# Optimization experiments

Hardware: AMD Instinct MI355X
Metric: run time of the kernel (lower is better)

The kernel has to match this reference:

```python
import jax, jax.numpy as jnp
import numpy as np
import math

B, M, DM = 8, 512, 1024
H, DH = 16, 64
DFF = 4096
RA, RF, RO = 32, 384, 384
EPS = 1e-12  # BERT LayerNorm eps


def layernorm(x, g, b):
    mu = jnp.mean(x, axis=-1, keepdims=True)
    var = jnp.mean(jnp.square(x - mu), axis=-1, keepdims=True)
    return (x - mu) * jax.lax.rsqrt(var + EPS) * g + b


def setup_inputs() -> dict:
    key = jax.random.key(0)
    ks = jax.random.split(key, 24)
    s = 0.02
    inp = {
        "x": jax.random.normal(ks[0], (B, M, DM), jnp.float32),
        "mask": jnp.zeros((B, M), jnp.float32),  # additive attention mask
        "Pq": jax.random.normal(ks[1], (H, DM, RA), jnp.float32) * s,
        "Vq": jax.random.normal(ks[2], (H, RA, DH), jnp.float32) * s,
        "Pk": jax.random.normal(ks[3], (H, DM, RA), jnp.float32) * s,
        "Vk": jax.random.normal(ks[4], (H, RA, DH), jnp.float32) * s,
        "Pv": jax.random.normal(ks[5], (H, DM, RA), jnp.float32) * s,
        "Vv": jax.random.normal(ks[6], (H, RA, DH), jnp.float32) * s,
        "bq": jax.random.normal(ks[7], (H, DH), jnp.float32) * s,
        "bk": jax.random.normal(ks[8], (H, DH), jnp.float32) * s,
        "bv": jax.random.normal(ks[9], (H, DH), jnp.float32) * s,
        "Uo": jax.random.normal(ks[10], (DM, RO), jnp.float32) * s,
        "Vo": jax.random.normal(ks[11], (RO, DM), jnp.float32) * s,
        "bo_attn": jax.random.normal(ks[12], (DM,), jnp.float32) * s,
        "U1": jax.random.normal(ks[13], (DM, RF), jnp.float32) * s,
        "V1": jax.random.normal(ks[14], (RF, DFF), jnp.float32) * s,
        "b1": jax.random.normal(ks[15], (DFF,), jnp.float32) * s,
        "U2": jax.random.normal(ks[16], (DFF, RF), jnp.float32) * s,
        "V2": jax.random.normal(ks[17], (RF, DM), jnp.float32) * s,
        "b2": jax.random.normal(ks[18], (DM,), jnp.float32) * s,
        "ln1_g": jnp.ones((DM,), jnp.float32),
        "ln1_b": jnp.zeros((DM,), jnp.float32),
        "ln2_g": jnp.ones((DM,), jnp.float32),
        "ln2_b": jnp.zeros((DM,), jnp.float32),
    }
    return inp


def reference(x, mask, Pq, Vq, Pk, Vk, Pv, Vv, bq, bk, bv,
              Uo, Vo, bo_attn, U1, V1, b1, U2, V2, b2,
              ln1_g, ln1_b, ln2_g, ln2_b):
    b_, m_, dm = x.shape
    h = Pq.shape[0]
    dh = dm // h
    # low-rank per-head projections: x -> [B,H,M,R] -> [B,H,M,dh]
    q = jnp.einsum('bmd,hdr->bhmr', x, Pq)
    k = jnp.einsum('bmd,hdr->bhmr', x, Pk)
    v = jnp.einsum('bmd,hdr->bhmr', x, Pv)
    Q = jnp.einsum('bhmr,hrd->bhmd', q, Vq) + bq[None, :, None, :]
    K = jnp.einsum('bhmr,hrd->bhmd', k, Vk) + bk[None, :, None, :]
    V = jnp.einsum('bhmr,hrd->bhmd', v, Vv) + bv[None, :, None, :]
    # scaled dot-product attention (flash_svd_attention equivalent)
    scores = jnp.einsum('bhmd,bhnd->bhmn', Q, K) / math.sqrt(dh)
    scores = scores + mask[:, None, None, :]
    probs = jax.nn.softmax(scores, axis=-1)
    attn = jnp.einsum('bhmn,bhnd->bhmd', probs, V)  # [B,H,M,dh]
    attn = attn.transpose(0, 2, 1, 3).reshape(b_, m_, dm)
    # low-rank output projection + residual + LN
    x1 = layernorm(x + (attn @ Uo) @ Vo + bo_attn, ln1_g, ln1_b)
    # flashsvd_ffn_v1 equivalent: gelu((x1 @ U1) @ V1 + b1) @ U2 @ V2 + b2
    mid = x1 @ U1
    hdn = jax.nn.gelu(mid @ V1 + b1, approximate=False)
    y = (hdn @ U2) @ V2 + b2
    out = layernorm(x1 + y, ln2_g, ln2_b)
    return out
```

## Files before the change

kernel.cpp:

```cpp
#include <hip/hip_runtime.h>
#include <math.h>

typedef __attribute__((ext_vector_type(8))) short short8;
typedef __attribute__((ext_vector_type(4))) float floatx4;

__device__ inline unsigned short f2bf(float f){
    union { float f; unsigned u; } v; v.f = f;
    unsigned r = v.u + 0x7fffu + ((v.u >> 16) & 1u);
    return (unsigned short)(r >> 16);
}
__device__ inline float bf2f(unsigned short b){
    union { unsigned u; float f; } v; v.u = ((unsigned)b) << 16;
    return v.f;
}
__device__ inline unsigned short to_bf(float f){ return f2bf(f); }
__device__ inline unsigned short to_bf(unsigned short u){ return u; }

#define GLD_LDS16(g, l) __builtin_amdgcn_global_load_lds( \
    (const __attribute__((address_space(1))) void*)(g),   \
    (__attribute__((address_space(3))) void*)(l), 16, 0, 0)

__global__ __launch_bounds__(256) void cast_kernel(const float* __restrict__ s,
                                                   unsigned short* __restrict__ d){
    int i = (blockIdx.x*256 + threadIdx.x)*4;
    float4 v = *(const float4*)(s+i);
    ushort4 o; o.x=f2bf(v.x); o.y=f2bf(v.y); o.z=f2bf(v.z); o.w=f2bf(v.w);
    *(ushort4*)(d+i) = o;
}

__global__ __launch_bounds__(256) void reduce4_kernel(
    const float* __restrict__ p, unsigned short* __restrict__ o, long mn){
    long i = ((long)blockIdx.x*256 + threadIdx.x)*4;
    float4 a = *(const float4*)(p+i);
    float4 b = *(const float4*)(p+mn+i);
    float4 c = *(const float4*)(p+2*mn+i);
    float4 d = *(const float4*)(p+3*mn+i);
    ushort4 r;
    r.x = f2bf(a.x+b.x+c.x+d.x); r.y = f2bf(a.y+b.y+c.y+d.y);
    r.z = f2bf(a.z+b.z+c.z+d.z); r.w = f2bf(a.w+b.w+c.w+d.w);
    *(ushort4*)(o+i) = r;
}

__global__ __launch_bounds__(256) void bcat_kernel(
    const float* __restrict__ bq, const float* __restrict__ bk,
    const float* __restrict__ bv, float* __restrict__ bcat){
    int i = blockIdx.x*256 + threadIdx.x;
    const float* p = (i < 1024) ? bq : (i < 2048) ? bk : bv;
    bcat[i] = p[i & 1023];
}

template<typename T>
__global__ __launch_bounds__(256) void trans_kernel(
    const T* __restrict__ src, unsigned short* __restrict__ dst,
    int R, int C, long sz, long dz)
{
    __shared__ unsigned short tile[32][33];
    const T* s = src + (size_t)blockIdx.z * sz;
    unsigned short* d = dst + (size_t)blockIdx.z * dz;
    int c0 = blockIdx.x*32, r0 = blockIdx.y*32;
    int tr = threadIdx.x>>3, tc = (threadIdx.x&7)*4;
    const T* sp = s + (size_t)(r0+tr)*C + c0 + tc;
#pragma unroll
    for (int i=0;i<4;i++) tile[tr][tc+i] = to_bf(sp[i]);
    __syncthreads();
    ushort4 o; o.x = tile[tc+0][tr]; o.y = tile[tc+1][tr];
    o.z = tile[tc+2][tr]; o.w = tile[tc+3][tr];
    *(ushort4*)(d + (size_t)(c0+tr)*R + r0 + tc) = o;
}

__global__ __launch_bounds__(256) void mm64_kernel(
    const unsigned short* __restrict__ A, const unsigned short* __restrict__ Bt,
    unsigned short* __restrict__ C, int Kdim, int lda, int ldb, int ldc,
    long ah, long al, long bh, long bl, long ch, long cl)
{
    __shared__ unsigned short As[64*40];
    __shared__ unsigned short Bs[64*40];
    int z = blockIdx.z;
    const unsigned short* Ab = A + (size_t)(z>>4)*ah + (size_t)(z&15)*al;
    const unsigned short* Bb = Bt + (size_t)(z>>4)*bh + (size_t)(z&15)*bl;
    int row0 = blockIdx.y*64, col0 = blockIdx.x*64;
    int t = threadIdx.x;
    int ar = t>>2, ak = (t&3)*8;
    int w = t>>6, lane = t&63, quad = lane>>4, c16 = lane&15;
    int wm = (w&1)*32, wn = (w>>1)*32;

    floatx4 zero = {0.f,0.f,0.f,0.f};
    floatx4 acc[2][2];
    acc[0][0]=zero; acc[0][1]=zero; acc[1][0]=zero; acc[1][1]=zero;

    const unsigned short* Ap = Ab + (size_t)(row0+ar)*lda + ak;
    const unsigned short* Bp = Bb + (size_t)(col0+ar)*ldb + ak;

    for (int kk=0; kk<Kdim; kk+=32){
        uint4 av = *(const uint4*)(Ap + kk);
        uint4 bv = *(const uint4*)(Bp + kk);
        __syncthreads();
        *(uint4*)(As + ar*40 + ak) = av;
        *(uint4*)(Bs + ar*40 + ak) = bv;
        __syncthreads();
        short8 a0 = *(const short8*)(As + (wm   +c16)*40 + quad*8);
        short8 a1 = *(const short8*)(As + (wm+16+c16)*40 + quad*8);
        short8 b0 = *(const short8*)(Bs + (wn   +c16)*40 + quad*8);
        short8 b1 = *(const short8*)(Bs + (wn+16+c16)*40 + quad*8);
        acc[0][0] = __builtin_amdgcn_mfma_f32_16x16x32_bf16(a0,b0,acc[0][0],0,0,0);
        acc[0][1] = __builtin_amdgcn_mfma_f32_16x16x32_bf16(a0,b1,acc[0][1],0,0,0);
        acc[1][0] = __builtin_amdgcn_mfma_f32_16x16x32_bf16(a1,b0,acc[1][0],0,0,0);
        acc[1][1] = __builtin_amdgcn_mfma_f32_16x16x32_bf16(a1,b1,acc[1][1],0,0,0);
    }

    size_t zc = (size_t)(z>>4)*ch + (size_t)(z&15)*cl;
#pragma unroll
    for (int mt=0; mt<2; mt++)
#pragma unroll
    for (int r=0; r<4; r++){
        int row = row0 + wm + mt*16 + quad*4 + r;
#pragma unroll
        for (int nt=0; nt<2; nt++){
            int col = col0 + wn + nt*16 + c16;
            C[zc + (size_t)row*ldc + col] = f2bf(acc[mt][nt][r]);
        }
    }
}

template<int EPI>
__global__ __launch_bounds__(256) void mm128_kernel(
    const unsigned short* __restrict__ A, const unsigned short* __restrict__ Bt,
    void* __restrict__ C, int Kdim, int lda, int ldb, int ldc,
    const float* __restrict__ aux, const float* __restrict__ resid)
{
    __shared__ unsigned short As[128*32];
    __shared__ unsigned short Bs[128*32];
    int row0 = blockIdx.y*128, col0 = blockIdx.x*128;
    int t = threadIdx.x;
    int w = t>>6, lane = t&63, quad = lane>>4, c16 = lane&15;
    int wm = (w&1)*64, wn = (w>>1)*64;

    int srow = w*32 + (lane>>2);
    int skcol = (lane&3)*8;
    unsigned short* AsW0 = As + (w*32)*32;
    unsigned short* AsW1 = As + (w*32+16)*32;
    unsigned short* BsW0 = Bs + (w*32)*32;
    unsigned short* BsW1 = Bs + (w*32+16)*32;
    const unsigned short* Ag0 = A + (size_t)(row0 + srow)*lda + skcol;
    const unsigned short* Ag1 = Ag0 + (size_t)16*lda;
    const unsigned short* Bg0 = Bt + (size_t)(col0 + srow)*ldb + skcol;
    const unsigned short* Bg1 = Bg0 + (size_t)16*ldb;

    floatx4 acc[4][4];
#pragma unroll
    for (int i=0;i<4;i++)
#pragma unroll
    for (int j=0;j<4;j++) acc[i][j] = (floatx4){0.f,0.f,0.f,0.f};

    for (int kk=0; kk<Kdim; kk+=32){
        GLD_LDS16(Ag0 + kk, AsW0);
        GLD_LDS16(Ag1 + kk, AsW1);
        GLD_LDS16(Bg0 + kk, BsW0);
        GLD_LDS16(Bg1 + kk, BsW1);
        __syncthreads();
        short8 a[4], b[4];
#pragma unroll
        for (int mt=0; mt<4; mt++)
            a[mt] = *(const short8*)(As + (wm + mt*16 + c16)*32 + quad*8);
#pragma unroll
        for (int nt=0; nt<4; nt++)
            b[nt] = *(const short8*)(Bs + (wn + nt*16 + c16)*32 + quad*8);
#pragma unroll
        for (int mt=0; mt<4; mt++)
#pragma unroll
            for (int nt=0; nt<4; nt++)
                acc[mt][nt] = __builtin_amdgcn_mfma_f32_16x16x32_bf16(
                    a[mt], b[nt], acc[mt][nt], 0,0,0);
        __syncthreads();
    }

#pragma unroll
    for (int mt=0; mt<4; mt++)
#pragma unroll
    for (int r=0; r<4; r++){
        int row = row0 + wm + mt*16 + quad*4 + r;
#pragma unroll
        for (int nt=0; nt<4; nt++){
            int col = col0 + wn + nt*16 + c16;
            float v = acc[mt][nt][r];
            if (EPI==0) {
                ((unsigned short*)C)[(size_t)row*ldc + col] = f2bf(v);
            } else if (EPI==2) {
                v += aux[col];
                v = 0.5f*v*(1.0f + erff(v*0.70710678118654752f));
                ((unsigned short*)C)[(size_t)row*ldc + col] = f2bf(v);
            } else if (EPI==3) {
                ((float*)C)[(size_t)row*ldc + col] =
                    v + aux[col] + resid[(size_t)row*ldc + col];
            } else {
                int proj = col >> 10, cw = col & 1023;
                int b_ = row >> 9, m_ = row & 511;
                size_t idx = (size_t)proj*4194304
                           + ((size_t)(b_*16 + (cw>>6))*512 + m_)*64 + (cw&63);
                ((unsigned short*)C)[idx] = f2bf(v + aux[col]);
            }
        }
    }
}

__global__ __launch_bounds__(256) void mmsk_kernel(
    const unsigned short* __restrict__ A, const unsigned short* __restrict__ Bt,
    float* __restrict__ Cp, int Kchunk, int lda, int ldb, int ldc, long mn)
{
    __shared__ unsigned short As[128*32];
    __shared__ unsigned short Bs[128*32];
    int row0 = blockIdx.y*128, col0 = blockIdx.x*128;
    int t = threadIdx.x;
    int w = t>>6, lane = t&63, quad = lane>>4, c16 = lane&15;
    int wm = (w&1)*64, wn = (w>>1)*64;

    int srow = w*32 + (lane>>2);
    int skcol = (lane&3)*8;
    unsigned short* AsW0 = As + (w*32)*32;
    unsigned short* AsW1 = As + (w*32+16)*32;
    unsigned short* BsW0 = Bs + (w*32)*32;
    unsigned short* BsW1 = Bs + (w*32+16)*32;
    const unsigned short* Ag0 = A + (size_t)(row0 + srow)*lda + skcol;
    const unsigned short* Ag1 = Ag0 + (size_t)16*lda;
    const unsigned short* Bg0 = Bt + (size_t)(col0 + srow)*ldb + skcol;
    const unsigned short* Bg1 = Bg0 + (size_t)16*ldb;

    floatx4 acc[4][4];
#pragma unroll
    for (int i=0;i<4;i++)
#pragma unroll
    for (int j=0;j<4;j++) acc[i][j] = (floatx4){0.f,0.f,0.f,0.f};

    int k0 = blockIdx.z * Kchunk;
    for (int kk=k0; kk<k0+Kchunk; kk+=32){
        GLD_LDS16(Ag0 + kk, AsW0);
        GLD_LDS16(Ag1 + kk, AsW1);
        GLD_LDS16(Bg0 + kk, BsW0);
        GLD_LDS16(Bg1 + kk, BsW1);
        __syncthreads();
        short8 a[4], b[4];
#pragma unroll
        for (int mt=0; mt<4; mt++)
            a[mt] = *(const short8*)(As + (wm + mt*16 + c16)*32 + quad*8);
#pragma unroll
        for (int nt=0; nt<4; nt++)
            b[nt] = *(const short8*)(Bs + (wn + nt*16 + c16)*32 + quad*8);
#pragma unroll
        for (int mt=0; mt<4; mt++)
#pragma unroll
            for (int nt=0; nt<4; nt++)
                acc[mt][nt] = __builtin_amdgcn_mfma_f32_16x16x32_bf16(
                    a[mt], b[nt], acc[mt][nt], 0,0,0);
        __syncthreads();
    }

    float* Cz = Cp + (size_t)blockIdx.z * mn;
#pragma unroll
    for (int mt=0; mt<4; mt++)
#pragma unroll
    for (int r=0; r<4; r++){
        int row = row0 + wm + mt*16 + quad*4 + r;
#pragma unroll
        for (int nt=0; nt<4; nt++){
            int col = col0 + wn + nt*16 + c16;
            Cz[(size_t)row*ldc + col] = acc[mt][nt][r];
        }
    }
}

__global__ __launch_bounds__(256) void flash_kernel(
    const unsigned short* __restrict__ Qb, const unsigned short* __restrict__ Kb,
    const unsigned short* __restrict__ Vt, const float* __restrict__ mask,
    unsigned short* __restrict__ attn)
{
    __shared__ unsigned short Qs[128*64];
    __shared__ unsigned short Ks[64*64];
    __shared__ unsigned short Vts[64*64];
    __shared__ unsigned short Ps[4][32*68];

    int qt = blockIdx.x, bh = blockIdx.y;
    int b = bh >> 4, h = bh & 15;
    int t = threadIdx.x;
    int w = t>>6, lane = t&63, quad = lane>>4, c16 = lane&15;

    const unsigned short* Qtile = Qb + ((size_t)bh*512 + qt*128)*64;
    const unsigned short* Ktile0 = Kb + (size_t)bh*512*64;
    const unsigned short* Vtbh = Vt + (size_t)bh*32768;

#pragma unroll
    for (int i=0;i<4;i++){
        GLD_LDS16(Qtile + (size_t)(w*32 + i*8)*64 + lane*8, Qs + (w*32+i*8)*64);
    }

    floatx4 Oacc[2][4];
#pragma unroll
    for (int mt=0;mt<2;mt++)
#pragma unroll
    for (int nd=0;nd<4;nd++) Oacc[mt][nd] = (floatx4){0.f,0.f,0.f,0.f};
    float mrow[2][4], lrow[2][4];
#pragma unroll
    for (int mt=0;mt<2;mt++)
#pragma unroll
    for (int r=0;r<4;r++){ mrow[mt][r] = -3.0e38f; lrow[mt][r] = 0.f; }

    unsigned short* Pw = &Ps[w][0];

    for (int kt=0; kt<8; kt++){
        __syncthreads();
#pragma unroll
        for (int i=0;i<2;i++){
            GLD_LDS16(Ktile0 + (size_t)(kt*64 + w*16 + i*8)*64 + lane*8,
                      Ks + (w*16+i*8)*64);
            GLD_LDS16(Vtbh + (size_t)(w*16 + i*8 + (lane>>3))*512 + kt*64 + (lane&7)*8,
                      Vts + (w*16+i*8)*64);
        }
        __syncthreads();

        floatx4 Sacc[2][4];
#pragma unroll
        for (int mt=0;mt<2;mt++)
#pragma unroll
        for (int nt=0;nt<4;nt++) Sacc[mt][nt] = (floatx4){0.f,0.f,0.f,0.f};
#pragma unroll
        for (int ks=0; ks<2; ks++){
            short8 a[2], bfr[4];
#pragma unroll
            for (int mt=0;mt<2;mt++)
                a[mt] = *(const short8*)(Qs + (w*32 + mt*16 + c16)*64 + ks*32 + quad*8);
#pragma unroll
            for (int nt=0;nt<4;nt++)
                bfr[nt] = *(const short8*)(Ks + (nt*16 + c16)*64 + ks*32 + quad*8);
#pragma unroll
            for (int mt=0;mt<2;mt++)
#pragma unroll
            for (int nt=0;nt<4;nt++)
                Sacc[mt][nt] = __builtin_amdgcn_mfma_f32_16x16x32_bf16(
                    a[mt], bfr[nt], Sacc[mt][nt], 0,0,0);
        }

        float mv[4];
#pragma unroll
        for (int nt=0;nt<4;nt++)
            mv[nt] = mask[b*512 + kt*64 + nt*16 + c16];

#pragma unroll
        for (int mt=0;mt<2;mt++)
#pragma unroll
        for (int r=0;r<4;r++){
            float sv[4];
#pragma unroll
            for (int nt=0;nt<4;nt++) sv[nt] = Sacc[mt][nt][r]*0.125f + mv[nt];
            float rmax = fmaxf(fmaxf(sv[0],sv[1]), fmaxf(sv[2],sv[3]));
            rmax = fmaxf(rmax, __shfl_xor(rmax, 1));
            rmax = fmaxf(rmax, __shfl_xor(rmax, 2));
            rmax = fmaxf(rmax, __shfl_xor(rmax, 4));
            rmax = fmaxf(rmax, __shfl_xor(rmax, 8));
            float mold = mrow[mt][r];
            float mnew = fmaxf(mold, rmax);
            float alpha = __expf(mold - mnew);
            float p[4], ps = 0.f;
#pragma unroll
            for (int nt=0;nt<4;nt++){ p[nt] = __expf(sv[nt]-mnew); ps += p[nt]; }
            ps += __shfl_xor(ps, 1);
            ps += __shfl_xor(ps, 2);
            ps += __shfl_xor(ps, 4);
            ps += __shfl_xor(ps, 8);
            lrow[mt][r] = lrow[mt][r]*alpha + ps;
            mrow[mt][r] = mnew;
#pragma unroll
            for (int nd=0;nd<4;nd++) Oacc[mt][nd][r] *= alpha;
#pragma unroll
            for (int nt=0;nt<4;nt++)
                Pw[(mt*16 + quad*4 + r)*68 + nt*16 + c16] = f2bf(p[nt]);
        }

#pragma unroll
        for (int ks=0; ks<2; ks++){
            short8 a[2], bfr[4];
#pragma unroll
            for (int mt=0;mt<2;mt++)
                a[mt] = *(const short8*)(Pw + (mt*16 + c16)*68 + ks*32 + quad*8);
#pragma unroll
            for (int nd=0;nd<4;nd++)
                bfr[nd] = *(const short8*)(Vts + (nd*16 + c16)*64 + ks*32 + quad*8);
#pragma unroll
            for (int mt=0;mt<2;mt++)
#pragma unroll
            for (int nd=0;nd<4;nd++)
                Oacc[mt][nd] = __builtin_amdgcn_mfma_f32_16x16x32_bf16(
                    a[mt], bfr[nd], Oacc[mt][nd], 0,0,0);
        }
    }

#pragma unroll
    for (int mt=0;mt<2;mt++)
#pragma unroll
    for (int r=0;r<4;r++){
        int m = qt*128 + w*32 + mt*16 + quad*4 + r;
        float inv = 1.0f / lrow[mt][r];
        unsigned short* op = attn + ((size_t)(b*512 + m))*1024 + h*64;
#pragma unroll
        for (int nd=0;nd<4;nd++)
            op[nd*16 + c16] = f2bf(Oacc[mt][nd][r] * inv);
    }
}

template<int DUAL>
__global__ __launch_bounds__(256) void ln_kernel(
    const float* __restrict__ in, const float* __restrict__ g,
    const float* __restrict__ bta, float* __restrict__ outf,
    unsigned short* __restrict__ outb)
{
    int row = blockIdx.x;
    int t = threadIdx.x;
    const float* x = in + (size_t)row*1024;
    float4 xv = ((const float4*)x)[t];
    float s  = xv.x + xv.y + xv.z + xv.w;
    float ss = xv.x*xv.x + xv.y*xv.y + xv.z*xv.z + xv.w*xv.w;
#pragma unroll
    for (int off=32; off>0; off>>=1){ s += __shfl_down(s, off); ss += __shfl_down(ss, off); }
    __shared__ float rs[4], rss[4];
    int wid = t>>6, lane = t&63;
    if (lane==0){ rs[wid]=s; rss[wid]=ss; }
    __syncthreads();
    s  = rs[0]+rs[1]+rs[2]+rs[3];
    ss = rss[0]+rss[1]+rss[2]+rss[3];
    float mu  = s * (1.0f/1024.0f);
    float var = ss * (1.0f/1024.0f) - mu*mu;
    float inv = rsqrtf(var + 1e-12f);
    float4 gv = ((const float4*)g)[t];
    float4 bv = ((const float4*)bta)[t];
    float4 o = make_float4((xv.x-mu)*inv*gv.x+bv.x, (xv.y-mu)*inv*gv.y+bv.y,
                           (xv.z-mu)*inv*gv.z+bv.z, (xv.w-mu)*inv*gv.w+bv.w);
    ((float4*)(outf + (size_t)row*1024))[t] = o;
    if (DUAL){
        ushort4 ob; ob.x=f2bf(o.x); ob.y=f2bf(o.y); ob.z=f2bf(o.z); ob.w=f2bf(o.w);
        ((ushort4*)(outb + (size_t)row*1024))[t] = ob;
    }
}

extern "C" void kernel_launch(void* const* d_in, const int* in_sizes, int n_in,
                              void* d_out, int out_size, void* d_ws, size_t ws_size,
                              hipStream_t stream)
{
    const float* x       = (const float*)d_in[0];
    const float* mask    = (const float*)d_in[1];
    const float* Pq      = (const float*)d_in[2];
    const float* Vq      = (const float*)d_in[3];
    const float* Pk      = (const float*)d_in[4];
    const float* Vk      = (const float*)d_in[5];
    const float* Pv      = (const float*)d_in[6];
    const float* Vv      = (const float*)d_in[7];
    const float* bq      = (const float*)d_in[8];
    const float* bk      = (const float*)d_in[9];
    const float* bv      = (const float*)d_in[10];
    const float* Uo      = (const float*)d_in[11];
    const float* Vo      = (const float*)d_in[12];
    const float* bo_attn = (const float*)d_in[13];
    const float* U1      = (const float*)d_in[14];
    const float* V1      = (const float*)d_in[15];
    const float* b1      = (const float*)d_in[16];
    const float* U2      = (const float*)d_in[17];
    const float* V2      = (const float*)d_in[18];
    const float* b2      = (const float*)d_in[19];
    const float* ln1_g   = (const float*)d_in[20];
    const float* ln1_b   = (const float*)d_in[21];
    const float* ln2_g   = (const float*)d_in[22];
    const float* ln2_b   = (const float*)d_in[23];
    float* out = (float*)d_out;

    char* base = (char*)d_ws;
    unsigned short* Uo_t   = (unsigned short*)(base + 0);
    unsigned short* Vo_t   = (unsigned short*)(base + 786432);
    unsigned short* U1_t   = (unsigned short*)(base + 1572864);
    unsigned short* V1_t   = (unsigned short*)(base + 2359296);
    unsigned short* U2_t   = (unsigned short*)(base + 5505024);
    unsigned short* V2_t   = (unsigned short*)(base + 8650752);
    float*          bcat   = (float*)(base + 9437184);
    unsigned short* Wt     = (unsigned short*)(base + 9449472);
    unsigned short* Pbf    = (unsigned short*)(base + 15740928);
    unsigned short* Vt2    = (unsigned short*)(base + 18886656);
    unsigned short* x_bf   = (unsigned short*)(base + 19083264);
    unsigned short* t_bf   = (unsigned short*)(base + 9449472);
    float*          ybuf   = (float*)(base + 12595200);
    float*          x1     = (float*)(base + 29372416);
    unsigned short* x1_bf  = (unsigned short*)(base + 46149632);
    unsigned short* hdn_bf = (unsigned short*)(base + 54538240);
    float*          part0  = (float*)(base + 12595200);
    float*          part1  = (float*)(base + 54538240);
    float*          part2  = (float*)(base + 88092672);
    unsigned short* Qb     = (unsigned short*)(base + 76558336);
    unsigned short* Kb     = (unsigned short*)(base + 84946944);
    unsigned short* Vb     = (unsigned short*)(base + 93535552);
    unsigned short* Vt     = (unsigned short*)(base + 101924160);
    unsigned short* attn_bf= (unsigned short*)(base + 110312768);

    const long MN384 = 4096L*384;

    cast_kernel<<<4096,256,0,stream>>>(x, x_bf);
    cast_kernel<<<512,256,0,stream>>>(Pq, Pbf);
    cast_kernel<<<512,256,0,stream>>>(Pk, Pbf + 524288);
    cast_kernel<<<512,256,0,stream>>>(Pv, Pbf + 1048576);
    trans_kernel<float><<<dim3(2,1,16),256,0,stream>>>(Vq, Vt2,           32,64, 2048,2048);
    trans_kernel<float><<<dim3(2,1,16),256,0,stream>>>(Vk, Vt2 + 32768,   32,64, 2048,2048);
    trans_kernel<float><<<dim3(2,1,16),256,0,stream>>>(Vv, Vt2 + 65536,   32,64, 2048,2048);
    bcat_kernel<<<12,256,0,stream>>>(bq, bk, bv, bcat);
    trans_kernel<float><<<dim3(12,32,1),256,0,stream>>>(Uo, Uo_t, 1024,384, 0,0);
    trans_kernel<float><<<dim3(32,12,1),256,0,stream>>>(Vo, Vo_t, 384,1024, 0,0);
    trans_kernel<float><<<dim3(12,32,1),256,0,stream>>>(U1, U1_t, 1024,384, 0,0);
    trans_kernel<float><<<dim3(128,12,1),256,0,stream>>>(V1, V1_t, 384,4096, 0,0);
    trans_kernel<float><<<dim3(12,128,1),256,0,stream>>>(U2, U2_t, 4096,384, 0,0);
    trans_kernel<float><<<dim3(32,12,1),256,0,stream>>>(V2, V2_t, 384,1024, 0,0);

    mm64_kernel<<<dim3(16,1,48),256,0,stream>>>(Vt2, Pbf, Wt,
        32, 32, 32, 1024, 32768,2048, 524288,32768, 1048576,65536);

    mm128_kernel<4><<<dim3(24,32,1),256,0,stream>>>(x_bf, Wt, Qb,
        1024, 1024, 1024, 3072, bcat, nullptr);

    trans_kernel<unsigned short><<<dim3(2,16,128),256,0,stream>>>(Vb, Vt, 512,64, 32768,32768);

    flash_kernel<<<dim3(4,128),256,0,stream>>>(Qb, Kb, Vt, mask, attn_bf);

    mmsk_kernel<<<dim3(3,32,4),256,0,stream>>>(attn_bf, Uo_t, part0,
        256, 1024, 1024, 384, MN384);
    reduce4_kernel<<<1536,256,0,stream>>>(part0, t_bf, MN384);
    mm128_kernel<3><<<dim3(8,32,1),256,0,stream>>>(t_bf, Vo_t, ybuf,
        384, 384, 384, 1024, bo_attn, x);
    ln_kernel<1><<<4096,256,0,stream>>>(ybuf, ln1_g, ln1_b, x1, x1_bf);
    mmsk_kernel<<<dim3(3,32,4),256,0,stream>>>(x1_bf, U1_t, part1,
        256, 1024, 1024, 384, MN384);
    reduce4_kernel<<<1536,256,0,stream>>>(part1, t_bf, MN384);
    mm128_kernel<2><<<dim3(32,32,1),256,0,stream>>>(t_bf, V1_t, hdn_bf,
        384, 384, 384, 4096, b1, nullptr);
    mmsk_kernel<<<dim3(3,32,4),256,0,stream>>>(hdn_bf, U2_t, part2,
        1024, 4096, 4096, 384, MN384);
    reduce4_kernel<<<1536,256,0,stream>>>(part2, t_bf, MN384);
    mm128_kernel<3><<<dim3(8,32,1),256,0,stream>>>(t_bf, V2_t, ybuf,
        384, 384, 384, 1024, b2, x1);
    ln_kernel<0><<<4096,256,0,stream>>>(ybuf, ln2_g, ln2_b, out, nullptr);
}
```

Baseline: 415.3 us.

## Double GEMM K-tile to 64 with XOR-swizzled LDS and batch prep kernels

The 128x128 MFMA GEMM kernels (mm128 and split-K mmsk) now stage a 64-wide K slice per iteration instead of 32. The LDS layout uses an XOR swizzle on 16-byte chunks to avoid bank conflicts, which halves the number of barrier pairs per K. Separately, several small weight cast and transpose launches are merged into combined kernels to cut launch overhead. The larger LDS footprint (32KB per block) may lower occupancy, and every K must be a multiple of 64.

```diff
diff --git a/kernel.cpp b/kernel.cpp
--- a/kernel.cpp
+++ b/kernel.cpp
@@ -26,6 +26,18 @@
     float4 v = *(const float4*)(s+i);
     ushort4 o; o.x=f2bf(v.x); o.y=f2bf(v.y); o.z=f2bf(v.z); o.w=f2bf(v.w);
     *(ushort4*)(d+i) = o;
+}
+
+__global__ __launch_bounds__(256) void castP_kernel(
+    const float* __restrict__ p0, const float* __restrict__ p1,
+    const float* __restrict__ p2, unsigned short* __restrict__ d){
+    int blk = blockIdx.x;
+    int proj = blk >> 9;
+    const float* s = (proj==0)?p0:(proj==1)?p1:p2;
+    int off = (blk & 511)*1024 + threadIdx.x*4;
+    float4 v = *(const float4*)(s+off);
+    ushort4 o; o.x=f2bf(v.x); o.y=f2bf(v.y); o.z=f2bf(v.z); o.w=f2bf(v.w);
+    *(ushort4*)(d + (size_t)proj*524288 + off) = o;
 }
 
 __global__ __launch_bounds__(256) void reduce4_kernel(
@@ -68,6 +80,45 @@
     *(ushort4*)(d + (size_t)(c0+tr)*R + r0 + tc) = o;
 }
 
+__global__ __launch_bounds__(256) void trans2_kernel(
+    const float* __restrict__ s0, unsigned short* __restrict__ d0,
+    const float* __restrict__ s1, unsigned short* __restrict__ d1,
+    int R, int C)
+{
+    __shared__ unsigned short tile[32][33];
+    const float* s = blockIdx.z ? s1 : s0;
+    unsigned short* d = blockIdx.z ? d1 : d0;
+    int c0 = blockIdx.x*32, r0 = blockIdx.y*32;
+    int tr = threadIdx.x>>3, tc = (threadIdx.x&7)*4;
+    const float* sp = s + (size_t)(r0+tr)*C + c0 + tc;
+#pragma unroll
+    for (int i=0;i<4;i++) tile[tr][tc+i] = f2bf(sp[i]);
+    __syncthreads();
+    ushort4 o; o.x = tile[tc+0][tr]; o.y = tile[tc+1][tr];
+    o.z = tile[tc+2][tr]; o.w = tile[tc+3][tr];
+    *(ushort4*)(d + (size_t)(c0+tr)*R + r0 + tc) = o;
+}
+
+__global__ __launch_bounds__(256) void vtrans3_kernel(
+    const float* __restrict__ v0, const float* __restrict__ v1,
+    const float* __restrict__ v2, unsigned short* __restrict__ dst)
+{
+    __shared__ unsigned short tile[32][33];
+    int z = blockIdx.z;
+    int proj = z >> 4, h = z & 15;
+    const float* s = ((proj==0)?v0:(proj==1)?v1:v2) + h*2048;
+    unsigned short* d = dst + (size_t)proj*32768 + h*2048;
+    int c0 = blockIdx.x*32;
+    int tr = threadIdx.x>>3, tc = (threadIdx.x&7)*4;
+    const float* sp = s + (size_t)tr*64 + c0 + tc;
+#pragma unroll
+    for (int i=0;i<4;i++) tile[tr][tc+i] = f2bf(sp[i]);
+    __syncthreads();
+    ushort4 o; o.x = tile[tc+0][tr]; o.y = tile[tc+1][tr];
+    o.z = tile[tc+2][tr]; o.w = tile[tc+3][tr];
+    *(ushort4*)(d + (size_t)(c0+tr)*32 + tc) = o;
+}
+
 __global__ __launch_bounds__(256) void mm64_kernel(
     const unsigned short* __restrict__ A, const unsigned short* __restrict__ Bt,
     unsigned short* __restrict__ C, int Kdim, int lda, int ldb, int ldc,
@@ -128,23 +179,19 @@
     void* __restrict__ C, int Kdim, int lda, int ldb, int ldc,
     const float* __restrict__ aux, const float* __restrict__ resid)
 {
-    __shared__ unsigned short As[128*32];
-    __shared__ unsigned short Bs[128*32];
+    __shared__ unsigned short As[128*64];
+    __shared__ unsigned short Bs[128*64];
     int row0 = blockIdx.y*128, col0 = blockIdx.x*128;
     int t = threadIdx.x;
     int w = t>>6, lane = t&63, quad = lane>>4, c16 = lane&15;
     int wm = (w&1)*64, wn = (w>>1)*64;
 
-    int srow = w*32 + (lane>>2);
-    int skcol = (lane&3)*8;
-    unsigned short* AsW0 = As + (w*32)*32;
-    unsigned short* AsW1 = As + (w*32+16)*32;
-    unsigned short* BsW0 = Bs + (w*32)*32;
-    unsigned short* BsW1 = Bs + (w*32+16)*32;
-    const unsigned short* Ag0 = A + (size_t)(row0 + srow)*lda + skcol;
-    const unsigned short* Ag1 = Ag0 + (size_t)16*lda;
-    const unsigned short* Bg0 = Bt + (size_t)(col0 + srow)*ldb + skcol;
-    const unsigned short* Bg1 = Bg0 + (size_t)16*ldb;
+    int srow = lane>>3;
+    int kc = (lane&7) ^ srow;
+    const unsigned short* Ag = A + (size_t)(row0 + w*32 + srow)*lda + kc*8;
+    const unsigned short* Bg = Bt + (size_t)(col0 + w*32 + srow)*ldb + kc*8;
+    unsigned short* AsW = As + (w*32)*64;
+    unsigned short* BsW = Bs + (w*32)*64;
 
     floatx4 acc[4][4];
 #pragma unroll
@@ -152,25 +199,33 @@
 #pragma unroll
     for (int j=0;j<4;j++) acc[i][j] = (floatx4){0.f,0.f,0.f,0.f};
 
-    for (int kk=0; kk<Kdim; kk+=32){
-        GLD_LDS16(Ag0 + kk, AsW0);
-        GLD_LDS16(Ag1 + kk, AsW1);
-        GLD_LDS16(Bg0 + kk, BsW0);
-        GLD_LDS16(Bg1 + kk, BsW1);
-        __syncthreads();
-        short8 a[4], b[4];
-#pragma unroll
-        for (int mt=0; mt<4; mt++)
-            a[mt] = *(const short8*)(As + (wm + mt*16 + c16)*32 + quad*8);
-#pragma unroll
-        for (int nt=0; nt<4; nt++)
-            b[nt] = *(const short8*)(Bs + (wn + nt*16 + c16)*32 + quad*8);
-#pragma unroll
-        for (int mt=0; mt<4; mt++)
+    int xa = (c16&7)*8;
+
+    for (int kk=0; kk<Kdim; kk+=64){
+#pragma unroll
+        for (int i=0;i<4;i++){
+            GLD_LDS16(Ag + (size_t)(i*8)*lda + kk, AsW + i*512);
+            GLD_LDS16(Bg + (size_t)(i*8)*ldb + kk, BsW + i*512);
+        }
+        __syncthreads();
+#pragma unroll
+        for (int ks=0; ks<2; ks++){
+            short8 a[4], b[4];
+#pragma unroll
+            for (int mt=0; mt<4; mt++)
+                a[mt] = *(const short8*)(As + (wm + mt*16 + c16)*64
+                                            + (((ks*4 + quad)*8) ^ xa));
 #pragma unroll
             for (int nt=0; nt<4; nt++)
-                acc[mt][nt] = __builtin_amdgcn_mfma_f32_16x16x32_bf16(
-                    a[mt], b[nt], acc[mt][nt], 0,0,0);
+                b[nt] = *(const short8*)(Bs + (wn + nt*16 + c16)*64
+                                            + (((ks*4 + quad)*8) ^ xa));
+#pragma unroll
+            for (int mt=0; mt<4; mt++)
+#pragma unroll
+                for (int nt=0; nt<4; nt++)
+                    acc[mt][nt] = __builtin_amdgcn_mfma_f32_16x16x32_bf16(
+                        a[mt], b[nt], acc[mt][nt], 0,0,0);
+        }
         __syncthreads();
     }
 
@@ -207,23 +262,19 @@
     const unsigned short* __restrict__ A, const unsigned short* __restrict__ Bt,
     float* __restrict__ Cp, int Kchunk, int lda, int ldb, int ldc, long mn)
 {
-    __shared__ unsigned short As[128*32];
-    __shared__ unsigned short Bs[128*32];
+    __shared__ unsigned short As[128*64];
+    __shared__ unsigned short Bs[128*64];
     int row0 = blockIdx.y*128, col0 = blockIdx.x*128;
     int t = threadIdx.x;
     int w = t>>6, lane = t&63, quad = lane>>4, c16 = lane&15;
     int wm = (w&1)*64, wn = (w>>1)*64;
 
-    int srow = w*32 + (lane>>2);
-    int skcol = (lane&3)*8;
-    unsigned short* AsW0 = As + (w*32)*32;
-    unsigned short* AsW1 = As + (w*32+16)*32;
-    unsigned short* BsW0 = Bs + (w*32)*32;
-    unsigned short* BsW1 = Bs + (w*32+16)*32;
-    const unsigned short* Ag0 = A + (size_t)(row0 + srow)*lda + skcol;
-    const unsigned short* Ag1 = Ag0 + (size_t)16*lda;
-    const unsigned short* Bg0 = Bt + (size_t)(col0 + srow)*ldb + skcol;
-    const unsigned short* Bg1 = Bg0 + (size_t)16*ldb;
+    int srow = lane>>3;
+    int kc = (lane&7) ^ srow;
+    const unsigned short* Ag = A + (size_t)(row0 + w*32 + srow)*lda + kc*8;
+    const unsigned short* Bg = Bt + (size_t)(col0 + w*32 + srow)*ldb + kc*8;
+    unsigned short* AsW = As + (w*32)*64;
+    unsigned short* BsW = Bs + (w*32)*64;
 
     floatx4 acc[4][4];
 #pragma unroll
@@ -231,26 +282,33 @@
 #pragma unroll
     for (int j=0;j<4;j++) acc[i][j] = (floatx4){0.f,0.f,0.f,0.f};
 
+    int xa = (c16&7)*8;
     int k0 = blockIdx.z * Kchunk;
-    for (int kk=k0; kk<k0+Kchunk; kk+=32){
-        GLD_LDS16(Ag0 + kk, AsW0);
-        GLD_LDS16(Ag1 + kk, AsW1);
-        GLD_LDS16(Bg0 + kk, BsW0);
-        GLD_LDS16(Bg1 + kk, BsW1);
-        __syncthreads();
-        short8 a[4], b[4];
-#pragma unroll
-        for (int mt=0; mt<4; mt++)
-            a[mt] = *(const short8*)(As + (wm + mt*16 + c16)*32 + quad*8);
-#pragma unroll
-        for (int nt=0; nt<4; nt++)
-            b[nt] = *(const short8*)(Bs + (wn + nt*16 + c16)*32 + quad*8);
-#pragma unroll
-        for (int mt=0; mt<4; mt++)
+    for (int kk=k0; kk<k0+Kchunk; kk+=64){
+#pragma unroll
+        for (int i=0;i<4;i++){
+            GLD_LDS16(Ag + (size_t)(i*8)*lda + kk, AsW + i*512);
+            GLD_LDS16(Bg + (size_t)(i*8)*ldb + kk, BsW + i*512);
+        }
+        __syncthreads();
+#pragma unroll
+        for (int ks=0; ks<2; ks++){
+            short8 a[4], b[4];
+#pragma unroll
+            for (int mt=0; mt<4; mt++)
+                a[mt] = *(const short8*)(As + (wm + mt*16 + c16)*64
+                                            + (((ks*4 + quad)*8) ^ xa));
 #pragma unroll
             for (int nt=0; nt<4; nt++)
-                acc[mt][nt] = __builtin_amdgcn_mfma_f32_16x16x32_bf16(
-                    a[mt], b[nt], acc[mt][nt], 0,0,0);
+                b[nt] = *(const short8*)(Bs + (wn + nt*16 + c16)*64
+                                            + (((ks*4 + quad)*8) ^ xa));
+#pragma unroll
+            for (int mt=0; mt<4; mt++)
+#pragma unroll
+                for (int nt=0; nt<4; nt++)
+                    acc[mt][nt] = __builtin_amdgcn_mfma_f32_16x16x32_bf16(
+                        a[mt], b[nt], acc[mt][nt], 0,0,0);
+        }
         __syncthreads();
     }
 
@@ -498,19 +556,13 @@
     const long MN384 = 4096L*384;
 
     cast_kernel<<<4096,256,0,stream>>>(x, x_bf);
-    cast_kernel<<<512,256,0,stream>>>(Pq, Pbf);
-    cast_kernel<<<512,256,0,stream>>>(Pk, Pbf + 524288);
-    cast_kernel<<<512,256,0,stream>>>(Pv, Pbf + 1048576);
-    trans_kernel<float><<<dim3(2,1,16),256,0,stream>>>(Vq, Vt2,           32,64, 2048,2048);
-    trans_kernel<float><<<dim3(2,1,16),256,0,stream>>>(Vk, Vt2 + 32768,   32,64, 2048,2048);
-    trans_kernel<float><<<dim3(2,1,16),256,0,stream>>>(Vv, Vt2 + 65536,   32,64, 2048,2048);
+    castP_kernel<<<1536,256,0,stream>>>(Pq, Pk, Pv, Pbf);
+    vtrans3_kernel<<<dim3(2,1,48),256,0,stream>>>(Vq, Vk, Vv, Vt2);
     bcat_kernel<<<12,256,0,stream>>>(bq, bk, bv, bcat);
-    trans_kernel<float><<<dim3(12,32,1),256,0,stream>>>(Uo, Uo_t, 1024,384, 0,0);
-    trans_kernel<float><<<dim3(32,12,1),256,0,stream>>>(Vo, Vo_t, 384,1024, 0,0);
-    trans_kernel<float><<<dim3(12,32,1),256,0,stream>>>(U1, U1_t, 1024,384, 0,0);
+    trans2_kernel<<<dim3(12,32,2),256,0,stream>>>(Uo, Uo_t, U1, U1_t, 1024, 384);
+    trans2_kernel<<<dim3(32,12,2),256,0,stream>>>(Vo, Vo_t, V2, V2_t, 384, 1024);
     trans_kernel<float><<<dim3(128,12,1),256,0,stream>>>(V1, V1_t, 384,4096, 0,0);
     trans_kernel<float><<<dim3(12,128,1),256,0,stream>>>(U2, U2_t, 4096,384, 0,0);
-    trans_kernel<float><<<dim3(32,12,1),256,0,stream>>>(V2, V2_t, 384,1024, 0,0);
 
     mm64_kernel<<<dim3(16,1,48),256,0,stream>>>(Vt2, Pbf, Wt,
         32, 32, 32, 1024, 32768,2048, 524288,32768, 1048576,65536);
```

After: 378.6 us. -8.8%, faster.
